# Optimization experiments

Measured on AMD Instinct MI355X. Metric: run time of the kernel, lower is better.

## Reference

```python
import jax, jax.numpy as jnp
import numpy as np

B, N, D = 8, 256, 3          # batch, particles, spatial dims
H = 64                        # hidden_nf (channels)
L = 4                         # num_layers
ENC = 3                       # atom_type, aa_type, aa_pos
IN_NF = ENC + 1               # + time
COORDS_RANGE = 15.0 / L       # tanh=True -> coords_range/n_layers
E = B * N * N                 # fully-connected edges per batch graph


def _linear(key, fin, fout):
    k1, k2 = jax.random.split(key)
    s = 1.0 / np.sqrt(fin)
    w = jax.random.uniform(k1, (fout, fin), minval=-s, maxval=s, dtype=jnp.float32)
    b = jax.random.uniform(k2, (fout,), minval=-s, maxval=s, dtype=jnp.float32)
    return w, b


def setup_inputs() -> dict:
    key = jax.random.key(0)
    ks = jax.random.split(key, 64)
    inp = {
        "t": jax.random.uniform(ks[0], (B, 1), dtype=jnp.float32),
        "x": jax.random.normal(ks[1], (B, N * D), dtype=jnp.float32),
        "atom_type": jax.random.uniform(ks[2], (B, N), dtype=jnp.float32),
        "aa_type": jax.random.uniform(ks[3], (B, N), dtype=jnp.float32),
        "aa_pos": jax.random.uniform(ks[4], (B, N), dtype=jnp.float32),
        "node_mask": jnp.ones((B, N), dtype=jnp.float32),
    }
    inp["emb_w"], inp["emb_b"] = _linear(ks[5], IN_NF, H)
    specs = [("edge_w1", "edge_b1", 2 * H + 2, H), ("edge_w2", "edge_b2", H, H),
             ("node_w1", "node_b1", 2 * H, H), ("node_w2", "node_b2", H, H),
             ("coord_w1", "coord_b1", H, H), ("att_w", "att_b", H, 1)]
    kk = 6
    for wn, bn, fin, fout in specs:
        ws, bs = [], []
        for _ in range(L):
            w, b = _linear(ks[kk], fin, fout); kk += 1
            ws.append(w); bs.append(b)
        inp[wn] = jnp.stack(ws); inp[bn] = jnp.stack(bs)
    # final coord layer: Linear(H,1,bias=False), xavier gain 0.001
    inp["coord_w2"] = jax.random.normal(ks[kk], (L, 1, H), dtype=jnp.float32) * 0.001
    return inp


def _edges():
    idx = jnp.arange(N)
    row_in = jnp.repeat(idx, N)
    col_in = jnp.tile(idx, N)
    off = (jnp.arange(B) * N)[:, None]
    row = (off + row_in[None, :]).reshape(-1)
    col = (off + col_in[None, :]).reshape(-1)
    return row, col


def reference(t, x, atom_type, aa_type, aa_pos, node_mask,
              emb_w, emb_b, edge_w1, edge_b1, edge_w2, edge_b2,
              node_w1, node_b1, node_w2, node_b2,
              coord_w1, coord_b1, att_w, att_b, coord_w2):
    silu = jax.nn.silu
    row, col = _edges()
    nm = node_mask.reshape(B * N, 1)
    # edge mask: pairwise node mask with diagonal (self-loop) removed
    em = ((node_mask[:, :, None] * node_mask[:, None, :])
          * (1.0 - jnp.eye(N, dtype=jnp.float32))).reshape(E, 1)

    x0 = x.reshape(B * N, D) * nm
    tt = jnp.broadcast_to(t, (B, N)).reshape(B * N, 1) * nm
    h = jnp.stack([atom_type, aa_type, aa_pos], axis=-1).reshape(B * N, ENC) * nm
    h = jnp.concatenate([h, tt], axis=1)                      # [BN, 4]
    edge_attr0 = jnp.sum((x0[row] - x0[col]) ** 2, axis=1, keepdims=True)  # [E,1]

    h = h @ emb_w.T + emb_b                                   # embedding -> [BN, H]
    coord = x0
    for l in range(L):
        diff = coord[row] - coord[col]                        # [E, D]
        radial = jnp.sum(diff ** 2, axis=1, keepdims=True)    # [E, 1]
        diff = diff / (jnp.sqrt(radial + 1e-8) + 1.0)         # norm_diff
        m = jnp.concatenate([h[row], h[col], radial, edge_attr0], axis=1)
        m = silu(m @ edge_w1[l].T + edge_b1[l])
        m = silu(m @ edge_w2[l].T + edge_b2[l])               # [E, H]
        m = m * jax.nn.sigmoid(m @ att_w[l].T + att_b[l]) * em
        phi = jnp.tanh(silu(m @ coord_w1[l].T + coord_b1[l]) @ coord_w2[l].T)
        trans = diff * phi * COORDS_RANGE * em                # [E, D]
        coord = (coord + jax.ops.segment_sum(trans, row, num_segments=B * N)) * nm
        agg = jax.ops.segment_sum(m, row, num_segments=B * N)  # [BN, H]
        upd = jnp.concatenate([h, agg], axis=1)
        upd = silu(upd @ node_w1[l].T + node_b1[l]) @ node_w2[l].T + node_b2[l]
        h = (h + upd) * nm                                    # recurrent residual

    vel = (coord - x0) * nm
    vel = vel.reshape(B, N, D)
    nmr = node_mask.reshape(B, N, 1)
    Ns = jnp.sum(nmr, axis=1, keepdims=True)
    vel = vel - (jnp.sum(vel, axis=1, keepdims=True) / Ns) * nmr  # remove_mean_with_mask
    return vel.reshape(B, N * D)
```

## Files before the change

kernel.cpp:

```cpp
#include <hip/hip_runtime.h>

#define CRANGE 3.75f

typedef _Float16 half_t;
typedef __attribute__((ext_vector_type(8))) _Float16 half8;
typedef __attribute__((ext_vector_type(4))) _Float16 half4;
typedef __attribute__((ext_vector_type(4))) float f32x4;

__device__ __forceinline__ float frcp(float x) { return __builtin_amdgcn_rcpf(x); }
__device__ __forceinline__ float fexpn(float x) { return __expf(fminf(x, 20.f)); }
__device__ __forceinline__ float fsilu(float x) { return x * frcp(1.f + fexpn(-x)); }

__device__ __forceinline__ void inv4(float d0, float d1, float d2, float d3, float* o) {
    float p01 = d0 * d1, p23 = d2 * d3;
    float r = frcp(p01 * p23);
    float t01 = p23 * r, t23 = p01 * r;
    o[0] = d1 * t01; o[1] = d0 * t01; o[2] = d3 * t23; o[3] = d2 * t23;
}
__device__ __forceinline__ void silu4(const float* x, float* o) {
    float d0 = 1.f + fexpn(-x[0]), d1 = 1.f + fexpn(-x[1]);
    float d2 = 1.f + fexpn(-x[2]), d3 = 1.f + fexpn(-x[3]);
    float iv[4]; inv4(d0, d1, d2, d3, iv);
    o[0] = x[0] * iv[0]; o[1] = x[1] * iv[1]; o[2] = x[2] * iv[2]; o[3] = x[3] * iv[3];
}

__global__ __launch_bounds__(256) void k_prepinit(
    const float* __restrict__ ew2, const float* __restrict__ cw1,
    const float* __restrict__ nw1, const float* __restrict__ nw2,
    const float* __restrict__ ew1,
    half_t* __restrict__ wf, float* __restrict__ trT,
    const float* __restrict__ t, const float* __restrict__ x,
    const float* __restrict__ at, const float* __restrict__ aa,
    const float* __restrict__ ap, const float* __restrict__ nm,
    const float* __restrict__ embw, const float* __restrict__ embb,
    const float* __restrict__ eb1_0,
    float* __restrict__ h, float* __restrict__ Hr, float* __restrict__ HcA,
    float* __restrict__ x0, float* __restrict__ cA)
{
    if (blockIdx.x < 336) {
        int idx = blockIdx.x * 256 + threadIdx.x;
        if (idx < 4096) {
            int lane = idx & 63;
            int g = (idx >> 6) & 7;
            int mat = (idx >> 9) & 1;
            int l = idx >> 10;
            int mt = g >> 1, kc = g & 1;
            int c = lane & 15, qq = lane >> 4;
            const float* W = (mat ? cw1 : ew2) + l * 4096;
            int row = 16 * mt + c;
            int k0 = 32 * kc + 8 * qq;
            half8 pk;
#pragma unroll
            for (int j = 0; j < 8; ++j) pk[j] = (half_t)W[row * 64 + k0 + j];
            ((half8*)wf)[idx] = pk;
        }
        int tid2 = idx - 4096;
        if (tid2 >= 0 && tid2 < 81920) {
            int l = tid2 / 20480, r = tid2 % 20480;
            float v;
            if (r < 8192)       { int k = r >> 6,        c = r & 63; v = nw1[l * 8192 + c * 128 + k]; }
            else if (r < 12288) { int r2 = r - 8192,  k = r2 >> 6, c = r2 & 63; v = nw2[l * 4096 + c * 64 + k]; }
            else if (r < 16384) { int r2 = r - 12288, k = r2 >> 6, c = r2 & 63; v = ew1[l * 8320 + c * 130 + k]; }
            else                { int r2 = r - 16384, k = r2 >> 6, c = r2 & 63; v = ew1[l * 8320 + c * 130 + 64 + k]; }
            trT[l * 20480 + r] = v;
        }
        return;
    }
    __shared__ float sh[4][64];
    int g = threadIdx.x >> 6, c = threadIdx.x & 63;
    int n = (blockIdx.x - 336) * 4 + g;
    float m = nm[n]; int b = n >> 8;
    float i0 = at[n] * m, i1 = aa[n] * m, i2 = ap[n] * m, i3 = t[b] * m;
    float4 w = ((const float4*)embw)[c];
    float hv = w.x * i0 + w.y * i1 + w.z * i2 + w.w * i3 + embb[c];
    sh[g][c] = hv; h[n * 64 + c] = hv;
    if (c < 3) { float v = x[n * 3 + c] * m; x0[n * 3 + c] = v; cA[n * 3 + c] = v; }
    __syncthreads();
    float a = eb1_0[c], bb = 0.f;
    const float* wa = ew1 + c * 130;
#pragma unroll
    for (int k = 0; k < 64; ++k) {
        float hk = sh[g][k];
        a  += wa[k] * hk;
        bb += wa[64 + k] * hk;
    }
    Hr[n * 64 + c] = a;
    HcA[n * 64 + c] = bb;
}

__global__ __launch_bounds__(256, 4) void k_edge(
    const float* __restrict__ coordIn, const float* __restrict__ x0,
    float* __restrict__ Hr, const float* __restrict__ Hc,
    const float* __restrict__ ew1, const float* __restrict__ eb2,
    const float* __restrict__ cb1, const float* __restrict__ attw,
    const float* __restrict__ attb, const float* __restrict__ cw2,
    const float* __restrict__ nm, const half_t* __restrict__ wf2,
    const half_t* __restrict__ wf1,
    float* __restrict__ hbuf,
    const float* __restrict__ nw1T, const float* __restrict__ nw2T,
    const float* __restrict__ nb1, const float* __restrict__ nb2,
    const float* __restrict__ ew1aTn, const float* __restrict__ ew1bTn,
    const float* __restrict__ eb1n,
    float* __restrict__ HcO, float* __restrict__ coordOut)
{
    __shared__ __align__(16) half_t sV[4][4096];
    __shared__ __align__(16) float sGeo[4][64][4];
    __shared__ float sHr[64], sWr[64], sWe[64], sB2[64], sBc1[64], sAttw[64], sWc2[64];
    __shared__ float sAgg[64];
    __shared__ float sCoord[3];

    const int i = blockIdx.x, b = i >> 8, ir = i & 255;
    const int t = threadIdx.x, wv = t >> 6, e = t & 63;
    const int q = e >> 4, c = e & 15;
    const int col = (b << 8) + t;

    if (t < 64) {
        sHr[t] = Hr[i * 64 + t];
        sWr[t] = ew1[t * 130 + 128];
        sWe[t] = ew1[t * 130 + 129];
        sB2[t] = eb2[t]; sBc1[t] = cb1[t]; sAttw[t] = attw[t]; sWc2[t] = cw2[t];
        sAgg[t] = 0.f;
    }
    if (t == 64) { sCoord[0] = 0.f; sCoord[1] = 0.f; sCoord[2] = 0.f; }
    float attb0 = attb[0];
    float nmi = nm[i];

    float dx = coordIn[i*3+0] - coordIn[col*3+0];
    float dy = coordIn[i*3+1] - coordIn[col*3+1];
    float dz = coordIn[i*3+2] - coordIn[col*3+2];
    float radial = dx*dx + dy*dy + dz*dz;
    float inv = frcp(__builtin_amdgcn_sqrtf(radial + 1e-8f) + 1.f);
    float ex = x0[i*3+0] - x0[col*3+0];
    float ey = x0[i*3+1] - x0[col*3+1];
    float ez = x0[i*3+2] - x0[col*3+2];
    float e0 = ex*ex + ey*ey + ez*ez;
    float em = nmi * nm[col] * ((t == ir) ? 0.f : 1.f);

    __syncthreads();

    {
        float4 g4 = make_float4(dx*inv, dy*inv, dz*inv, em);
        *(float4*)&sGeo[wv][e][0] = g4;
    }

    half_t* mybuf = (half_t*)sV[wv];
    const float4* hcv = (const float4*)(Hc + col * 64);
#pragma unroll
    for (int s = 0; s < 8; ++s) {
        float4 ha = hcv[2*s], hb = hcv[2*s+1];
        float z[8], so[8];
        z[0]=ha.x; z[1]=ha.y; z[2]=ha.z; z[3]=ha.w;
        z[4]=hb.x; z[5]=hb.y; z[6]=hb.z; z[7]=hb.w;
#pragma unroll
        for (int u = 0; u < 8; ++u) {
            int k = 8*s + u;
            z[u] = sHr[k] + z[u] + radial * sWr[k] + e0 * sWe[k];
        }
        silu4(z, so); silu4(z + 4, so + 4);
        half8 pk;
#pragma unroll
        for (int u = 0; u < 8; ++u) pk[u] = (half_t)so[u];
        int f = q * 2 + (s >> 2);
        *(half8*)&mybuf[f * 512 + ((s & 3) * 16 + c) * 8] = pk;
    }

    const half8* bv = (const half8*)mybuf;
    f32x4 acc[4][4];
#pragma unroll
    for (int mt = 0; mt < 4; ++mt) {
        int row0 = 16*mt + 4*q;
#pragma unroll
        for (int nt = 0; nt < 4; ++nt)
#pragma unroll
            for (int r = 0; r < 4; ++r) acc[mt][nt][r] = sB2[row0 + r];
    }
    {
        const half8* a2v = (const half8*)wf2;
        half8 a2[8];
#pragma unroll
        for (int g = 0; g < 8; ++g) a2[g] = a2v[g * 64 + e];
#pragma unroll
        for (int nt = 0; nt < 4; ++nt) {
            half8 b0 = bv[(nt*2+0)*64 + e];
            half8 b1 = bv[(nt*2+1)*64 + e];
#pragma unroll
            for (int mt = 0; mt < 4; ++mt) {
                acc[mt][nt] = __builtin_amdgcn_mfma_f32_16x16x32_f16(a2[mt*2+0], b0, acc[mt][nt], 0, 0, 0);
                acc[mt][nt] = __builtin_amdgcn_mfma_f32_16x16x32_f16(a2[mt*2+1], b1, acc[mt][nt], 0, 0, 0);
            }
        }
    }

    float attp[4] = {0.f, 0.f, 0.f, 0.f};
#pragma unroll
    for (int mt = 0; mt < 4; ++mt) {
        int row0 = 16*mt + 4*q;
#pragma unroll
        for (int nt = 0; nt < 4; ++nt) {
            float z[4], so[4];
#pragma unroll
            for (int r = 0; r < 4; ++r) z[r] = acc[mt][nt][r];
            silu4(z, so);
#pragma unroll
            for (int r = 0; r < 4; ++r) {
                acc[mt][nt][r] = so[r];
                attp[nt] += so[r] * sAttw[row0 + r];
            }
        }
    }
#pragma unroll
    for (int nt = 0; nt < 4; ++nt) {
        float v = attp[nt];
        v += __shfl_xor(v, 16);
        v += __shfl_xor(v, 32);
        attp[nt] = v;
    }
    float scale[4];
    {
        float d0 = 1.f + fexpn(-(attp[0] + attb0));
        float d1 = 1.f + fexpn(-(attp[1] + attb0));
        float d2 = 1.f + fexpn(-(attp[2] + attb0));
        float d3 = 1.f + fexpn(-(attp[3] + attb0));
        float iv[4]; inv4(d0, d1, d2, d3, iv);
#pragma unroll
        for (int nt = 0; nt < 4; ++nt) scale[nt] = iv[nt] * sGeo[wv][16*nt + c][3];
    }

    float aggp[4][4];
#pragma unroll
    for (int mt = 0; mt < 4; ++mt)
#pragma unroll
        for (int r = 0; r < 4; ++r) aggp[mt][r] = 0.f;
#pragma unroll
    for (int mt = 0; mt < 4; ++mt) {
        int kbase = 16*mt + 4*q;
        int fof = ((kbase >> 5) * 512) + (((kbase >> 3) & 3) * 128) + (kbase & 7);
#pragma unroll
        for (int nt = 0; nt < 4; ++nt) {
            half4 pk;
#pragma unroll
            for (int r = 0; r < 4; ++r) {
                float v = acc[mt][nt][r] * scale[nt];
                aggp[mt][r] += v;
                pk[r] = (half_t)v;
            }
            *(half4*)&mybuf[nt*1024 + fof + c*8] = pk;
        }
    }

    half8 a1[8];
    {
        const half8* a1v = (const half8*)wf1;
#pragma unroll
        for (int g = 0; g < 8; ++g) a1[g] = a1v[g * 64 + e];
    }

#pragma unroll
    for (int mt = 0; mt < 4; ++mt)
#pragma unroll
        for (int r = 0; r < 4; ++r) {
            float v = aggp[mt][r];
            v += __shfl_xor(v, 1); v += __shfl_xor(v, 2);
            v += __shfl_xor(v, 4); v += __shfl_xor(v, 8);
            if (c == 0) atomicAdd(&sAgg[16*mt + 4*q + r], v);
        }

    f32x4 acc2[4][4];
#pragma unroll
    for (int mt = 0; mt < 4; ++mt) {
        int row0 = 16*mt + 4*q;
#pragma unroll
        for (int nt = 0; nt < 4; ++nt)
#pragma unroll
            for (int r = 0; r < 4; ++r) acc2[mt][nt][r] = sBc1[row0 + r];
    }
#pragma unroll
    for (int nt = 0; nt < 4; ++nt) {
        half8 b0 = bv[(nt*2+0)*64 + e];
        half8 b1 = bv[(nt*2+1)*64 + e];
#pragma unroll
        for (int mt = 0; mt < 4; ++mt) {
            acc2[mt][nt] = __builtin_amdgcn_mfma_f32_16x16x32_f16(a1[mt*2+0], b0, acc2[mt][nt], 0, 0, 0);
            acc2[mt][nt] = __builtin_amdgcn_mfma_f32_16x16x32_f16(a1[mt*2+1], b1, acc2[mt][nt], 0, 0, 0);
        }
    }

    float php[4] = {0.f, 0.f, 0.f, 0.f};
#pragma unroll
    for (int mt = 0; mt < 4; ++mt) {
        int row0 = 16*mt + 4*q;
#pragma unroll
        for (int nt = 0; nt < 4; ++nt) {
            float z[4], so[4];
#pragma unroll
            for (int r = 0; r < 4; ++r) z[r] = acc2[mt][nt][r];
            silu4(z, so);
#pragma unroll
            for (int r = 0; r < 4; ++r) php[nt] += so[r] * sWc2[row0 + r];
        }
    }
#pragma unroll
    for (int nt = 0; nt < 4; ++nt) {
        float v = php[nt];
        v += __shfl_xor(v, 16);
        v += __shfl_xor(v, 32);
        php[nt] = v;
    }
    float tnh[4];
    {
        float d0 = fexpn(2.f * php[0]) + 1.f;
        float d1 = fexpn(2.f * php[1]) + 1.f;
        float d2 = fexpn(2.f * php[2]) + 1.f;
        float d3 = fexpn(2.f * php[3]) + 1.f;
        float iv[4]; inv4(d0, d1, d2, d3, iv);
#pragma unroll
        for (int nt = 0; nt < 4; ++nt) tnh[nt] = 1.f - 2.f * iv[nt];
    }
    float tx = 0.f, ty = 0.f, tz = 0.f;
#pragma unroll
    for (int nt = 0; nt < 4; ++nt) {
        float4 g4 = *(float4*)&sGeo[wv][16*nt + c][0];
        float tr = tnh[nt] * CRANGE * g4.w;
        tx += g4.x * tr; ty += g4.y * tr; tz += g4.z * tr;
    }
    tx += __shfl_xor(tx, 1); tx += __shfl_xor(tx, 2); tx += __shfl_xor(tx, 4); tx += __shfl_xor(tx, 8);
    ty += __shfl_xor(ty, 1); ty += __shfl_xor(ty, 2); ty += __shfl_xor(ty, 4); ty += __shfl_xor(ty, 8);
    tz += __shfl_xor(tz, 1); tz += __shfl_xor(tz, 2); tz += __shfl_xor(tz, 4); tz += __shfl_xor(tz, 8);
    if (e == 0) {
        atomicAdd(&sCoord[0], tx);
        atomicAdd(&sCoord[1], ty);
        atomicAdd(&sCoord[2], tz);
    }

    __syncthreads();

    float* sT  = (float*)&sV[0][0];
    float* sIn = sT;
    float* sU  = sT + 128;
    float* sHn = sT + 192;

    if (t < 64) sIn[t] = hbuf[i * 64 + t];
    else if (t < 128) sIn[t] = sAgg[t - 64];
    if (t >= 128 && t < 131) {
        int d = t - 128;
        coordOut[i * 3 + d] = (coordIn[i * 3 + d] + sCoord[d]) * nmi;
    }
    __syncthreads();

    const int o = (wv << 4) + c;
    {
        float a = 0.f;
        const float* w = nw1T + (q * 32) * 64 + o;
#pragma unroll
        for (int k = 0; k < 32; ++k) a += w[k * 64] * sIn[q * 32 + k];
        a += __shfl_xor(a, 16);
        a += __shfl_xor(a, 32);
        if (q == 0) sU[o] = fsilu(a + nb1[o]);
    }
    __syncthreads();
    {
        float a = 0.f;
        const float* w = nw2T + (q * 16) * 64 + o;
#pragma unroll
        for (int k = 0; k < 16; ++k) a += w[k * 64] * sU[q * 16 + k];
        a += __shfl_xor(a, 16);
        a += __shfl_xor(a, 32);
        if (q == 0) {
            float hn = (sIn[o] + a + nb2[o]) * nmi;
            hbuf[i * 64 + o] = hn;
            sHn[o] = hn;
        }
    }
    __syncthreads();
    {
        float a = 0.f, bb = 0.f;
        const float* wa = ew1aTn + (q * 16) * 64 + o;
        const float* wb = ew1bTn + (q * 16) * 64 + o;
#pragma unroll
        for (int k = 0; k < 16; ++k) {
            float hv = sHn[q * 16 + k];
            a  += wa[k * 64] * hv;
            bb += wb[k * 64] * hv;
        }
        a  += __shfl_xor(a, 16);  a  += __shfl_xor(a, 32);
        bb += __shfl_xor(bb, 16); bb += __shfl_xor(bb, 32);
        if (q == 0) {
            Hr[i * 64 + o]  = a + eb1n[o];
            HcO[i * 64 + o] = bb;
        }
    }
}

__global__ void k_final(const float* __restrict__ coord, const float* __restrict__ x0,
                        const float* __restrict__ nm, float* __restrict__ out) {
    int b = blockIdx.x;
    int t = threadIdx.x;
    int i = b * 256 + t;
    int lane = t & 63;
    float m = nm[i];
    float vx = (coord[i * 3 + 0] - x0[i * 3 + 0]) * m;
    float vy = (coord[i * 3 + 1] - x0[i * 3 + 1]) * m;
    float vz = (coord[i * 3 + 2] - x0[i * 3 + 2]) * m;
    __shared__ float red[4];
    if (t < 4) red[t] = 0.f;
    __syncthreads();
    float sx = vx, sy = vy, sz = vz, sn = m;
#pragma unroll
    for (int off = 1; off < 64; off <<= 1) {
        sx += __shfl_xor(sx, off);
        sy += __shfl_xor(sy, off);
        sz += __shfl_xor(sz, off);
        sn += __shfl_xor(sn, off);
    }
    if (lane == 0) {
        atomicAdd(&red[0], sx); atomicAdd(&red[1], sy);
        atomicAdd(&red[2], sz); atomicAdd(&red[3], sn);
    }
    __syncthreads();
    float invNs = frcp(red[3]);
    out[b * 768 + t * 3 + 0] = vx - red[0] * invNs * m;
    out[b * 768 + t * 3 + 1] = vy - red[1] * invNs * m;
    out[b * 768 + t * 3 + 2] = vz - red[2] * invNs * m;
}

extern "C" void kernel_launch(void* const* d_in, const int* in_sizes, int n_in,
                              void* d_out, int out_size, void* d_ws, size_t ws_size,
                              hipStream_t stream) {
    const float* t_in    = (const float*)d_in[0];
    const float* x_in    = (const float*)d_in[1];
    const float* at_in   = (const float*)d_in[2];
    const float* aa_in   = (const float*)d_in[3];
    const float* ap_in   = (const float*)d_in[4];
    const float* nm_in   = (const float*)d_in[5];
    const float* emb_w   = (const float*)d_in[6];
    const float* emb_b   = (const float*)d_in[7];
    const float* edge_w1 = (const float*)d_in[8];
    const float* edge_b1 = (const float*)d_in[9];
    const float* edge_w2 = (const float*)d_in[10];
    const float* edge_b2 = (const float*)d_in[11];
    const float* node_w1 = (const float*)d_in[12];
    const float* node_b1 = (const float*)d_in[13];
    const float* node_w2 = (const float*)d_in[14];
    const float* node_b2 = (const float*)d_in[15];
    const float* coord_w1= (const float*)d_in[16];
    const float* coord_b1= (const float*)d_in[17];
    const float* att_w   = (const float*)d_in[18];
    const float* att_b   = (const float*)d_in[19];
    const float* coord_w2= (const float*)d_in[20];

    float* ws  = (float*)d_ws;
    float* h   = ws;
    float* Hr  = h + 131072;
    float* HcA = Hr + 131072;
    float* HcB = HcA + 131072;
    float* x0  = HcB + 131072;
    float* cA  = x0 + 6144;
    float* cB  = cA + 6144;
    float* base = cB + 6144;
    half_t* wf = (half_t*)base;
    float* trT = base + 16384;

    float* out = (float*)d_out;

    k_prepinit<<<848, 256, 0, stream>>>(edge_w2, coord_w1, node_w1, node_w2, edge_w1,
                                        wf, trT,
                                        t_in, x_in, at_in, aa_in, ap_in, nm_in,
                                        emb_w, emb_b, edge_b1,
                                        h, Hr, HcA, x0, cA);

    for (int l = 0; l < 4; ++l) {
        const float* ew1 = edge_w1 + l * 8320;
        const float* eb2 = edge_b2 + l * 64;
        const float* cb1 = coord_b1 + l * 64;
        const float* aw  = att_w + l * 64;
        const float* ab  = att_b + l;
        const float* cw2 = coord_w2 + l * 64;
        const float* nb1 = node_b1 + l * 64;
        const float* nb2 = node_b2 + l * 64;

        const float* trL = trT + l * 20480;
        int ln = (l + 1) & 3;
        const float* trN = trT + ln * 20480;

        const float* cin  = (l & 1) ? cB : cA;
        float*       cout = (l & 1) ? cA : cB;
        const float* HcR  = (l & 1) ? HcB : HcA;
        float*       HcW  = (l & 1) ? HcA : HcB;

        k_edge<<<2048, 256, 0, stream>>>(cin, x0, Hr, HcR, ew1, eb2, cb1,
                                         aw, ab, cw2, nm_in,
                                         wf + l * 8192, wf + l * 8192 + 4096,
                                         h, trL, trL + 8192, nb1, nb2,
                                         trN + 12288, trN + 16384, edge_b1 + ln * 64,
                                         HcW, cout);
    }

    k_final<<<8, 256, 0, stream>>>(cA, x0, nm_in, out);
}
```

Before: 309.6 us.

## Fuse per-layer edge kernels and final reduction into one persistent kernel with grid barriers

Replaces the four per-layer edge launches and the final kernel with one persistent kernel. Its grid is sized from occupancy, it loops over nodes and separates phases with atomic grid barriers. The node update is split out into its own phase after a barrier, with aggregated messages staged through global memory instead of shared memory. The aim is to remove launch overhead between layers. In exchange it adds grid-barrier spin costs and an extra global round trip for agg, and it relies on every block being co-resident to avoid deadlock.

```diff
diff --git a/kernel.cpp b/kernel.cpp
--- a/kernel.cpp
+++ b/kernel.cpp
@@ -24,19 +24,43 @@
     o[0] = x[0] * iv[0]; o[1] = x[1] * iv[1]; o[2] = x[2] * iv[2]; o[3] = x[3] * iv[3];
 }
 
+struct MP {
+    const float* x0; float* cA; float* cB;
+    float* Hr; float* Hc; float* h; float* agg;
+    const float* ew1; const float* eb1; const float* eb2; const float* cb1;
+    const float* attw; const float* attb; const float* cw2; const float* nm;
+    const half_t* wf; const float* trT;
+    const float* nb1; const float* nb2;
+    float* out; int* bar; int nblk;
+};
+
+__device__ __forceinline__ void gridbar(int* cnt, int nblk) {
+    __syncthreads();
+    if (threadIdx.x == 0) {
+        __threadfence();
+        int arrived = __hip_atomic_fetch_add(cnt, 1, __ATOMIC_ACQ_REL, __HIP_MEMORY_SCOPE_AGENT) + 1;
+        if (arrived < nblk) {
+            while (__hip_atomic_load(cnt, __ATOMIC_ACQUIRE, __HIP_MEMORY_SCOPE_AGENT) < nblk)
+                __builtin_amdgcn_s_sleep(2);
+        }
+    }
+    __syncthreads();
+}
+
 __global__ __launch_bounds__(256) void k_prepinit(
     const float* __restrict__ ew2, const float* __restrict__ cw1,
     const float* __restrict__ nw1, const float* __restrict__ nw2,
     const float* __restrict__ ew1,
-    half_t* __restrict__ wf, float* __restrict__ trT,
+    half_t* __restrict__ wf, float* __restrict__ trT, int* __restrict__ bar,
     const float* __restrict__ t, const float* __restrict__ x,
     const float* __restrict__ at, const float* __restrict__ aa,
     const float* __restrict__ ap, const float* __restrict__ nm,
     const float* __restrict__ embw, const float* __restrict__ embb,
     const float* __restrict__ eb1_0,
-    float* __restrict__ h, float* __restrict__ Hr, float* __restrict__ HcA,
+    float* __restrict__ h, float* __restrict__ Hr, float* __restrict__ Hc,
     float* __restrict__ x0, float* __restrict__ cA)
 {
+    if (blockIdx.x == 0 && threadIdx.x < 16) bar[threadIdx.x] = 0;
     if (blockIdx.x < 336) {
         int idx = blockIdx.x * 256 + threadIdx.x;
         if (idx < 4096) {
@@ -85,23 +109,10 @@
         bb += wa[64 + k] * hk;
     }
     Hr[n * 64 + c] = a;
-    HcA[n * 64 + c] = bb;
+    Hc[n * 64 + c] = bb;
 }
 
-__global__ __launch_bounds__(256, 4) void k_edge(
-    const float* __restrict__ coordIn, const float* __restrict__ x0,
-    float* __restrict__ Hr, const float* __restrict__ Hc,
-    const float* __restrict__ ew1, const float* __restrict__ eb2,
-    const float* __restrict__ cb1, const float* __restrict__ attw,
-    const float* __restrict__ attb, const float* __restrict__ cw2,
-    const float* __restrict__ nm, const half_t* __restrict__ wf2,
-    const half_t* __restrict__ wf1,
-    float* __restrict__ hbuf,
-    const float* __restrict__ nw1T, const float* __restrict__ nw2T,
-    const float* __restrict__ nb1, const float* __restrict__ nb2,
-    const float* __restrict__ ew1aTn, const float* __restrict__ ew1bTn,
-    const float* __restrict__ eb1n,
-    float* __restrict__ HcO, float* __restrict__ coordOut)
+__global__ __launch_bounds__(256, 4) void k_mega(MP p)
 {
     __shared__ __align__(16) half_t sV[4][4096];
     __shared__ __align__(16) float sGeo[4][64][4];
@@ -109,318 +120,354 @@
     __shared__ float sAgg[64];
     __shared__ float sCoord[3];
 
-    const int i = blockIdx.x, b = i >> 8, ir = i & 255;
     const int t = threadIdx.x, wv = t >> 6, e = t & 63;
     const int q = e >> 4, c = e & 15;
-    const int col = (b << 8) + t;
-
-    if (t < 64) {
-        sHr[t] = Hr[i * 64 + t];
-        sWr[t] = ew1[t * 130 + 128];
-        sWe[t] = ew1[t * 130 + 129];
-        sB2[t] = eb2[t]; sBc1[t] = cb1[t]; sAttw[t] = attw[t]; sWc2[t] = cw2[t];
-        sAgg[t] = 0.f;
+
+    for (int l = 0; l < 4; ++l) {
+        const float* ew1l = p.ew1 + l * 8320;
+        const float* eb2l = p.eb2 + l * 64;
+        const float* cb1l = p.cb1 + l * 64;
+        const float* awl  = p.attw + l * 64;
+        const float  attb0 = p.attb[l];
+        const float* cw2l = p.cw2 + l * 64;
+        const half_t* wf2 = p.wf + l * 8192;
+        const half_t* wf1 = p.wf + l * 8192 + 4096;
+        const float* coordIn  = (l & 1) ? p.cB : p.cA;
+        float*       coordOut = (l & 1) ? p.cA : p.cB;
+
+        for (int i = blockIdx.x; i < 2048; i += gridDim.x) {
+            const int b = i >> 8, ir = i & 255;
+            const int col = (b << 8) + t;
+
+            if (t < 64) {
+                sHr[t] = p.Hr[i * 64 + t];
+                sWr[t] = ew1l[t * 130 + 128];
+                sWe[t] = ew1l[t * 130 + 129];
+                sB2[t] = eb2l[t]; sBc1[t] = cb1l[t]; sAttw[t] = awl[t]; sWc2[t] = cw2l[t];
+                sAgg[t] = 0.f;
+            }
+            if (t == 64) { sCoord[0] = 0.f; sCoord[1] = 0.f; sCoord[2] = 0.f; }
+            float nmi = p.nm[i];
+
+            float dx = coordIn[i*3+0] - coordIn[col*3+0];
+            float dy = coordIn[i*3+1] - coordIn[col*3+1];
+            float dz = coordIn[i*3+2] - coordIn[col*3+2];
+            float radial = dx*dx + dy*dy + dz*dz;
+            float inv = frcp(__builtin_amdgcn_sqrtf(radial + 1e-8f) + 1.f);
+            float ex = p.x0[i*3+0] - p.x0[col*3+0];
+            float ey = p.x0[i*3+1] - p.x0[col*3+1];
+            float ez = p.x0[i*3+2] - p.x0[col*3+2];
+            float e0 = ex*ex + ey*ey + ez*ez;
+            float em = nmi * p.nm[col] * ((t == ir) ? 0.f : 1.f);
+
+            __syncthreads();
+
+            {
+                float4 g4 = make_float4(dx*inv, dy*inv, dz*inv, em);
+                *(float4*)&sGeo[wv][e][0] = g4;
+            }
+
+            half_t* mybuf = (half_t*)sV[wv];
+            const float4* hcv = (const float4*)(p.Hc + col * 64);
+#pragma unroll
+            for (int s = 0; s < 8; ++s) {
+                float4 ha = hcv[2*s], hb = hcv[2*s+1];
+                float z[8], so[8];
+                z[0]=ha.x; z[1]=ha.y; z[2]=ha.z; z[3]=ha.w;
+                z[4]=hb.x; z[5]=hb.y; z[6]=hb.z; z[7]=hb.w;
+#pragma unroll
+                for (int u = 0; u < 8; ++u) {
+                    int k = 8*s + u;
+                    z[u] = sHr[k] + z[u] + radial * sWr[k] + e0 * sWe[k];
+                }
+                silu4(z, so); silu4(z + 4, so + 4);
+                half8 pk;
+#pragma unroll
+                for (int u = 0; u < 8; ++u) pk[u] = (half_t)so[u];
+                int f = q * 2 + (s >> 2);
+                *(half8*)&mybuf[f * 512 + ((s & 3) * 16 + c) * 8] = pk;
+            }
+
+            const half8* bv = (const half8*)mybuf;
+            f32x4 acc[4][4];
+#pragma unroll
+            for (int mt = 0; mt < 4; ++mt) {
+                int row0 = 16*mt + 4*q;
+#pragma unroll
+                for (int nt = 0; nt < 4; ++nt)
+#pragma unroll
+                    for (int r = 0; r < 4; ++r) acc[mt][nt][r] = sB2[row0 + r];
+            }
+            {
+                const half8* a2v = (const half8*)wf2;
+                half8 a2[8];
+#pragma unroll
+                for (int g = 0; g < 8; ++g) a2[g] = a2v[g * 64 + e];
+#pragma unroll
+                for (int nt = 0; nt < 4; ++nt) {
+                    half8 b0 = bv[(nt*2+0)*64 + e];
+                    half8 b1 = bv[(nt*2+1)*64 + e];
+#pragma unroll
+                    for (int mt = 0; mt < 4; ++mt) {
+                        acc[mt][nt] = __builtin_amdgcn_mfma_f32_16x16x32_f16(a2[mt*2+0], b0, acc[mt][nt], 0, 0, 0);
+                        acc[mt][nt] = __builtin_amdgcn_mfma_f32_16x16x32_f16(a2[mt*2+1], b1, acc[mt][nt], 0, 0, 0);
+                    }
+                }
+            }
+
+            float attp[4] = {0.f, 0.f, 0.f, 0.f};
+#pragma unroll
+            for (int mt = 0; mt < 4; ++mt) {
+                int row0 = 16*mt + 4*q;
+#pragma unroll
+                for (int nt = 0; nt < 4; ++nt) {
+                    float z[4], so[4];
+#pragma unroll
+                    for (int r = 0; r < 4; ++r) z[r] = acc[mt][nt][r];
+                    silu4(z, so);
+#pragma unroll
+                    for (int r = 0; r < 4; ++r) {
+                        acc[mt][nt][r] = so[r];
+                        attp[nt] += so[r] * sAttw[row0 + r];
+                    }
+                }
+            }
+#pragma unroll
+            for (int nt = 0; nt < 4; ++nt) {
+                float v = attp[nt];
+                v += __shfl_xor(v, 16);
+                v += __shfl_xor(v, 32);
+                attp[nt] = v;
+            }
+            float scale[4];
+            {
+                float d0 = 1.f + fexpn(-(attp[0] + attb0));
+                float d1 = 1.f + fexpn(-(attp[1] + attb0));
+                float d2 = 1.f + fexpn(-(attp[2] + attb0));
+                float d3 = 1.f + fexpn(-(attp[3] + attb0));
+                float iv[4]; inv4(d0, d1, d2, d3, iv);
+#pragma unroll
+                for (int nt = 0; nt < 4; ++nt) scale[nt] = iv[nt] * sGeo[wv][16*nt + c][3];
+            }
+
+            float aggp[4][4];
+#pragma unroll
+            for (int mt = 0; mt < 4; ++mt)
+#pragma unroll
+                for (int r = 0; r < 4; ++r) aggp[mt][r] = 0.f;
+#pragma unroll
+            for (int mt = 0; mt < 4; ++mt) {
+                int kbase = 16*mt + 4*q;
+                int fof = ((kbase >> 5) * 512) + (((kbase >> 3) & 3) * 128) + (kbase & 7);
+#pragma unroll
+                for (int nt = 0; nt < 4; ++nt) {
+                    half4 pk;
+#pragma unroll
+                    for (int r = 0; r < 4; ++r) {
+                        float v = acc[mt][nt][r] * scale[nt];
+                        aggp[mt][r] += v;
+                        pk[r] = (half_t)v;
+                    }
+                    *(half4*)&mybuf[nt*1024 + fof + c*8] = pk;
+                }
+            }
+
+            half8 a1[8];
+            {
+                const half8* a1v = (const half8*)wf1;
+#pragma unroll
+                for (int g = 0; g < 8; ++g) a1[g] = a1v[g * 64 + e];
+            }
+
+#pragma unroll
+            for (int mt = 0; mt < 4; ++mt)
+#pragma unroll
+                for (int r = 0; r < 4; ++r) {
+                    float v = aggp[mt][r];
+                    v += __shfl_xor(v, 1); v += __shfl_xor(v, 2);
+                    v += __shfl_xor(v, 4); v += __shfl_xor(v, 8);
+                    if (c == 0) atomicAdd(&sAgg[16*mt + 4*q + r], v);
+                }
+
+            f32x4 acc2[4][4];
+#pragma unroll
+            for (int mt = 0; mt < 4; ++mt) {
+                int row0 = 16*mt + 4*q;
+#pragma unroll
+                for (int nt = 0; nt < 4; ++nt)
+#pragma unroll
+                    for (int r = 0; r < 4; ++r) acc2[mt][nt][r] = sBc1[row0 + r];
+            }
+#pragma unroll
+            for (int nt = 0; nt < 4; ++nt) {
+                half8 b0 = bv[(nt*2+0)*64 + e];
+                half8 b1 = bv[(nt*2+1)*64 + e];
+#pragma unroll
+                for (int mt = 0; mt < 4; ++mt) {
+                    acc2[mt][nt] = __builtin_amdgcn_mfma_f32_16x16x32_f16(a1[mt*2+0], b0, acc2[mt][nt], 0, 0, 0);
+                    acc2[mt][nt] = __builtin_amdgcn_mfma_f32_16x16x32_f16(a1[mt*2+1], b1, acc2[mt][nt], 0, 0, 0);
+                }
+            }
+
+            float php[4] = {0.f, 0.f, 0.f, 0.f};
+#pragma unroll
+            for (int mt = 0; mt < 4; ++mt) {
+                int row0 = 16*mt + 4*q;
+#pragma unroll
+                for (int nt = 0; nt < 4; ++nt) {
+                    float z[4], so[4];
+#pragma unroll
+                    for (int r = 0; r < 4; ++r) z[r] = acc2[mt][nt][r];
+                    silu4(z, so);
+#pragma unroll
+                    for (int r = 0; r < 4; ++r) php[nt] += so[r] * sWc2[row0 + r];
+                }
+            }
+#pragma unroll
+            for (int nt = 0; nt < 4; ++nt) {
+                float v = php[nt];
+                v += __shfl_xor(v, 16);
+                v += __shfl_xor(v, 32);
+                php[nt] = v;
+            }
+            float tnh[4];
+            {
+                float d0 = fexpn(2.f * php[0]) + 1.f;
+                float d1 = fexpn(2.f * php[1]) + 1.f;
+                float d2 = fexpn(2.f * php[2]) + 1.f;
+                float d3 = fexpn(2.f * php[3]) + 1.f;
+                float iv[4]; inv4(d0, d1, d2, d3, iv);
+#pragma unroll
+                for (int nt = 0; nt < 4; ++nt) tnh[nt] = 1.f - 2.f * iv[nt];
+            }
+            float tx = 0.f, ty = 0.f, tz = 0.f;
+#pragma unroll
+            for (int nt = 0; nt < 4; ++nt) {
+                float4 g4 = *(float4*)&sGeo[wv][16*nt + c][0];
+                float tr = tnh[nt] * CRANGE * g4.w;
+                tx += g4.x * tr; ty += g4.y * tr; tz += g4.z * tr;
+            }
+            tx += __shfl_xor(tx, 1); tx += __shfl_xor(tx, 2); tx += __shfl_xor(tx, 4); tx += __shfl_xor(tx, 8);
+            ty += __shfl_xor(ty, 1); ty += __shfl_xor(ty, 2); ty += __shfl_xor(ty, 4); ty += __shfl_xor(ty, 8);
+            tz += __shfl_xor(tz, 1); tz += __shfl_xor(tz, 2); tz += __shfl_xor(tz, 4); tz += __shfl_xor(tz, 8);
+            if (e == 0) {
+                atomicAdd(&sCoord[0], tx);
+                atomicAdd(&sCoord[1], ty);
+                atomicAdd(&sCoord[2], tz);
+            }
+
+            __syncthreads();
+            if (t < 64) p.agg[i * 64 + t] = sAgg[t];
+            if (t >= 64 && t < 67) {
+                int d = t - 64;
+                coordOut[i * 3 + d] = (coordIn[i * 3 + d] + sCoord[d]) * nmi;
+            }
+            __syncthreads();
+        }
+
+        gridbar(p.bar + 2 * l, p.nblk);
+
+        if (l < 3) {
+            const float* trL = p.trT + l * 20480;
+            const float* trN = p.trT + (l + 1) * 20480;
+            const float* nw1T = trL;
+            const float* nw2T = trL + 8192;
+            const float* e1aT = trN + 12288;
+            const float* e1bT = trN + 16384;
+            const float* nb1l = p.nb1 + l * 64;
+            const float* nb2l = p.nb2 + l * 64;
+            const float* eb1n = p.eb1 + (l + 1) * 64;
+
+            float* sT  = (float*)&sV[0][0];
+            float* sIn = sT;
+            float* sP  = sT + 128;
+            float* sU  = sT + 384;
+            float* sHn = sT + 448;
+            float* sPB = sT + 512;
+            const int cc = t & 63, pp = t >> 6;
+
+            for (int n = blockIdx.x; n < 2048; n += gridDim.x) {
+                float nmi = p.nm[n];
+                if (t < 64) sIn[t] = p.h[n * 64 + t];
+                else if (t < 128) sIn[t] = p.agg[n * 64 + t - 64];
+                __syncthreads();
+                {
+                    float a = 0.f;
+                    const float* w = nw1T + (pp * 32) * 64 + cc;
+#pragma unroll
+                    for (int k = 0; k < 32; ++k) a += w[k * 64] * sIn[pp * 32 + k];
+                    sP[pp * 64 + cc] = a;
+                }
+                __syncthreads();
+                if (t < 64) sU[t] = fsilu(sP[t] + sP[64 + t] + sP[128 + t] + sP[192 + t] + nb1l[t]);
+                __syncthreads();
+                {
+                    float a = 0.f;
+                    const float* w = nw2T + (pp * 16) * 64 + cc;
+#pragma unroll
+                    for (int k = 0; k < 16; ++k) a += w[k * 64] * sU[pp * 16 + k];
+                    sP[pp * 64 + cc] = a;
+                }
+                __syncthreads();
+                if (t < 64) {
+                    float hn = (sIn[t] + sP[t] + sP[64 + t] + sP[128 + t] + sP[192 + t] + nb2l[t]) * nmi;
+                    p.h[n * 64 + t] = hn;
+                    sHn[t] = hn;
+                }
+                __syncthreads();
+                {
+                    float a = 0.f, b2 = 0.f;
+                    const float* wa = e1aT + (pp * 16) * 64 + cc;
+                    const float* wb = e1bT + (pp * 16) * 64 + cc;
+#pragma unroll
+                    for (int k = 0; k < 16; ++k) {
+                        float hv = sHn[pp * 16 + k];
+                        a  += wa[k * 64] * hv;
+                        b2 += wb[k * 64] * hv;
+                    }
+                    sP[pp * 64 + cc] = a;
+                    sPB[pp * 64 + cc] = b2;
+                }
+                __syncthreads();
+                if (t < 64) {
+                    p.Hr[n * 64 + t] = sP[t] + sP[64 + t] + sP[128 + t] + sP[192 + t] + eb1n[t];
+                    p.Hc[n * 64 + t] = sPB[t] + sPB[64 + t] + sPB[128 + t] + sPB[192 + t];
+                }
+                __syncthreads();
+            }
+            gridbar(p.bar + 2 * l + 1, p.nblk);
+        }
     }
-    if (t == 64) { sCoord[0] = 0.f; sCoord[1] = 0.f; sCoord[2] = 0.f; }
-    float attb0 = attb[0];
-    float nmi = nm[i];
-
-    float dx = coordIn[i*3+0] - coordIn[col*3+0];
-    float dy = coordIn[i*3+1] - coordIn[col*3+1];
-    float dz = coordIn[i*3+2] - coordIn[col*3+2];
-    float radial = dx*dx + dy*dy + dz*dz;
-    float inv = frcp(__builtin_amdgcn_sqrtf(radial + 1e-8f) + 1.f);
-    float ex = x0[i*3+0] - x0[col*3+0];
-    float ey = x0[i*3+1] - x0[col*3+1];
-    float ez = x0[i*3+2] - x0[col*3+2];
-    float e0 = ex*ex + ey*ey + ez*ez;
-    float em = nmi * nm[col] * ((t == ir) ? 0.f : 1.f);
-
-    __syncthreads();
-
-    {
-        float4 g4 = make_float4(dx*inv, dy*inv, dz*inv, em);
-        *(float4*)&sGeo[wv][e][0] = g4;
+
+    if (blockIdx.x < 8) {
+        float* red = (float*)&sV[0][0];
+        int b = blockIdx.x;
+        int i = b * 256 + t;
+        int lane = t & 63;
+        float m = p.nm[i];
+        float vx = (p.cA[i * 3 + 0] - p.x0[i * 3 + 0]) * m;
+        float vy = (p.cA[i * 3 + 1] - p.x0[i * 3 + 1]) * m;
+        float vz = (p.cA[i * 3 + 2] - p.x0[i * 3 + 2]) * m;
+        if (t < 4) red[t] = 0.f;
+        __syncthreads();
+        float sx = vx, sy = vy, sz = vz, sn = m;
+#pragma unroll
+        for (int off = 1; off < 64; off <<= 1) {
+            sx += __shfl_xor(sx, off);
+            sy += __shfl_xor(sy, off);
+            sz += __shfl_xor(sz, off);
+            sn += __shfl_xor(sn, off);
+        }
+        if (lane == 0) {
+            atomicAdd(&red[0], sx); atomicAdd(&red[1], sy);
+            atomicAdd(&red[2], sz); atomicAdd(&red[3], sn);
+        }
+        __syncthreads();
+        float invNs = frcp(red[3]);
+        p.out[b * 768 + t * 3 + 0] = vx - red[0] * invNs * m;
+        p.out[b * 768 + t * 3 + 1] = vy - red[1] * invNs * m;
+        p.out[b * 768 + t * 3 + 2] = vz - red[2] * invNs * m;
     }
-
-    half_t* mybuf = (half_t*)sV[wv];
-    const float4* hcv = (const float4*)(Hc + col * 64);
-#pragma unroll
-    for (int s = 0; s < 8; ++s) {
-        float4 ha = hcv[2*s], hb = hcv[2*s+1];
-        float z[8], so[8];
-        z[0]=ha.x; z[1]=ha.y; z[2]=ha.z; z[3]=ha.w;
-        z[4]=hb.x; z[5]=hb.y; z[6]=hb.z; z[7]=hb.w;
-#pragma unroll
-        for (int u = 0; u < 8; ++u) {
-            int k = 8*s + u;
-            z[u] = sHr[k] + z[u] + radial * sWr[k] + e0 * sWe[k];
-        }
-        silu4(z, so); silu4(z + 4, so + 4);
-        half8 pk;
-#pragma unroll
-        for (int u = 0; u < 8; ++u) pk[u] = (half_t)so[u];
-        int f = q * 2 + (s >> 2);
-        *(half8*)&mybuf[f * 512 + ((s & 3) * 16 + c) * 8] = pk;
-    }
-
-    const half8* bv = (const half8*)mybuf;
-    f32x4 acc[4][4];
-#pragma unroll
-    for (int mt = 0; mt < 4; ++mt) {
-        int row0 = 16*mt + 4*q;
-#pragma unroll
-        for (int nt = 0; nt < 4; ++nt)
-#pragma unroll
-            for (int r = 0; r < 4; ++r) acc[mt][nt][r] = sB2[row0 + r];
-    }
-    {
-        const half8* a2v = (const half8*)wf2;
-        half8 a2[8];
-#pragma unroll
-        for (int g = 0; g < 8; ++g) a2[g] = a2v[g * 64 + e];
-#pragma unroll
-        for (int nt = 0; nt < 4; ++nt) {
-            half8 b0 = bv[(nt*2+0)*64 + e];
-            half8 b1 = bv[(nt*2+1)*64 + e];
-#pragma unroll
-            for (int mt = 0; mt < 4; ++mt) {
-                acc[mt][nt] = __builtin_amdgcn_mfma_f32_16x16x32_f16(a2[mt*2+0], b0, acc[mt][nt], 0, 0, 0);
-                acc[mt][nt] = __builtin_amdgcn_mfma_f32_16x16x32_f16(a2[mt*2+1], b1, acc[mt][nt], 0, 0, 0);
-            }
-        }
-    }
-
-    float attp[4] = {0.f, 0.f, 0.f, 0.f};
-#pragma unroll
-    for (int mt = 0; mt < 4; ++mt) {
-        int row0 = 16*mt + 4*q;
-#pragma unroll
-        for (int nt = 0; nt < 4; ++nt) {
-            float z[4], so[4];
-#pragma unroll
-            for (int r = 0; r < 4; ++r) z[r] = acc[mt][nt][r];
-            silu4(z, so);
-#pragma unroll
-            for (int r = 0; r < 4; ++r) {
-                acc[mt][nt][r] = so[r];
-                attp[nt] += so[r] * sAttw[row0 + r];
-            }
-        }
-    }
-#pragma unroll
-    for (int nt = 0; nt < 4; ++nt) {
-        float v = attp[nt];
-        v += __shfl_xor(v, 16);
-        v += __shfl_xor(v, 32);
-        attp[nt] = v;
-    }
-    float scale[4];
-    {
-        float d0 = 1.f + fexpn(-(attp[0] + attb0));
-        float d1 = 1.f + fexpn(-(attp[1] + attb0));
-        float d2 = 1.f + fexpn(-(attp[2] + attb0));
-        float d3 = 1.f + fexpn(-(attp[3] + attb0));
-        float iv[4]; inv4(d0, d1, d2, d3, iv);
-#pragma unroll
-        for (int nt = 0; nt < 4; ++nt) scale[nt] = iv[nt] * sGeo[wv][16*nt + c][3];
-    }
-
-    float aggp[4][4];
-#pragma unroll
-    for (int mt = 0; mt < 4; ++mt)
-#pragma unroll
-        for (int r = 0; r < 4; ++r) aggp[mt][r] = 0.f;
-#pragma unroll
-    for (int mt = 0; mt < 4; ++mt) {
-        int kbase = 16*mt + 4*q;
-        int fof = ((kbase >> 5) * 512) + (((kbase >> 3) & 3) * 128) + (kbase & 7);
-#pragma unroll
-        for (int nt = 0; nt < 4; ++nt) {
-            half4 pk;
-#pragma unroll
-            for (int r = 0; r < 4; ++r) {
-                float v = acc[mt][nt][r] * scale[nt];
-                aggp[mt][r] += v;
-                pk[r] = (half_t)v;
-            }
-            *(half4*)&mybuf[nt*1024 + fof + c*8] = pk;
-        }
-    }
-
-    half8 a1[8];
-    {
-        const half8* a1v = (const half8*)wf1;
-#pragma unroll
-        for (int g = 0; g < 8; ++g) a1[g] = a1v[g * 64 + e];
-    }
-
-#pragma unroll
-    for (int mt = 0; mt < 4; ++mt)
-#pragma unroll
-        for (int r = 0; r < 4; ++r) {
-            float v = aggp[mt][r];
-            v += __shfl_xor(v, 1); v += __shfl_xor(v, 2);
-            v += __shfl_xor(v, 4); v += __shfl_xor(v, 8);
-            if (c == 0) atomicAdd(&sAgg[16*mt + 4*q + r], v);
-        }
-
-    f32x4 acc2[4][4];
-#pragma unroll
-    for (int mt = 0; mt < 4; ++mt) {
-        int row0 = 16*mt + 4*q;
-#pragma unroll
-        for (int nt = 0; nt < 4; ++nt)
-#pragma unroll
-            for (int r = 0; r < 4; ++r) acc2[mt][nt][r] = sBc1[row0 + r];
-    }
-#pragma unroll
-    for (int nt = 0; nt < 4; ++nt) {
-        half8 b0 = bv[(nt*2+0)*64 + e];
-        half8 b1 = bv[(nt*2+1)*64 + e];
-#pragma unroll
-        for (int mt = 0; mt < 4; ++mt) {
-            acc2[mt][nt] = __builtin_amdgcn_mfma_f32_16x16x32_f16(a1[mt*2+0], b0, acc2[mt][nt], 0, 0, 0);
-            acc2[mt][nt] = __builtin_amdgcn_mfma_f32_16x16x32_f16(a1[mt*2+1], b1, acc2[mt][nt], 0, 0, 0);
-        }
-    }
-
-    float php[4] = {0.f, 0.f, 0.f, 0.f};
-#pragma unroll
-    for (int mt = 0; mt < 4; ++mt) {
-        int row0 = 16*mt + 4*q;
-#pragma unroll
-        for (int nt = 0; nt < 4; ++nt) {
-            float z[4], so[4];
-#pragma unroll
-            for (int r = 0; r < 4; ++r) z[r] = acc2[mt][nt][r];
-            silu4(z, so);
-#pragma unroll
-            for (int r = 0; r < 4; ++r) php[nt] += so[r] * sWc2[row0 + r];
-        }
-    }
-#pragma unroll
-    for (int nt = 0; nt < 4; ++nt) {
-        float v = php[nt];
-        v += __shfl_xor(v, 16);
-        v += __shfl_xor(v, 32);
-        php[nt] = v;
-    }
-    float tnh[4];
-    {
-        float d0 = fexpn(2.f * php[0]) + 1.f;
-        float d1 = fexpn(2.f * php[1]) + 1.f;
-        float d2 = fexpn(2.f * php[2]) + 1.f;
-        float d3 = fexpn(2.f * php[3]) + 1.f;
-        float iv[4]; inv4(d0, d1, d2, d3, iv);
-#pragma unroll
-        for (int nt = 0; nt < 4; ++nt) tnh[nt] = 1.f - 2.f * iv[nt];
-    }
-    float tx = 0.f, ty = 0.f, tz = 0.f;
-#pragma unroll
-    for (int nt = 0; nt < 4; ++nt) {
-        float4 g4 = *(float4*)&sGeo[wv][16*nt + c][0];
-        float tr = tnh[nt] * CRANGE * g4.w;
-        tx += g4.x * tr; ty += g4.y * tr; tz += g4.z * tr;
-    }
-    tx += __shfl_xor(tx, 1); tx += __shfl_xor(tx, 2); tx += __shfl_xor(tx, 4); tx += __shfl_xor(tx, 8);
-    ty += __shfl_xor(ty, 1); ty += __shfl_xor(ty, 2); ty += __shfl_xor(ty, 4); ty += __shfl_xor(ty, 8);
-    tz += __shfl_xor(tz, 1); tz += __shfl_xor(tz, 2); tz += __shfl_xor(tz, 4); tz += __shfl_xor(tz, 8);
-    if (e == 0) {
-        atomicAdd(&sCoord[0], tx);
-        atomicAdd(&sCoord[1], ty);
-        atomicAdd(&sCoord[2], tz);
-    }
-
-    __syncthreads();
-
-    float* sT  = (float*)&sV[0][0];
-    float* sIn = sT;
-    float* sU  = sT + 128;
-    float* sHn = sT + 192;
-
-    if (t < 64) sIn[t] = hbuf[i * 64 + t];
-    else if (t < 128) sIn[t] = sAgg[t - 64];
-    if (t >= 128 && t < 131) {
-        int d = t - 128;
-        coordOut[i * 3 + d] = (coordIn[i * 3 + d] + sCoord[d]) * nmi;
-    }
-    __syncthreads();
-
-    const int o = (wv << 4) + c;
-    {
-        float a = 0.f;
-        const float* w = nw1T + (q * 32) * 64 + o;
-#pragma unroll
-        for (int k = 0; k < 32; ++k) a += w[k * 64] * sIn[q * 32 + k];
-        a += __shfl_xor(a, 16);
-        a += __shfl_xor(a, 32);
-        if (q == 0) sU[o] = fsilu(a + nb1[o]);
-    }
-    __syncthreads();
-    {
-        float a = 0.f;
-        const float* w = nw2T + (q * 16) * 64 + o;
-#pragma unroll
-        for (int k = 0; k < 16; ++k) a += w[k * 64] * sU[q * 16 + k];
-        a += __shfl_xor(a, 16);
-        a += __shfl_xor(a, 32);
-        if (q == 0) {
-            float hn = (sIn[o] + a + nb2[o]) * nmi;
-            hbuf[i * 64 + o] = hn;
-            sHn[o] = hn;
-        }
-    }
-    __syncthreads();
-    {
-        float a = 0.f, bb = 0.f;
-        const float* wa = ew1aTn + (q * 16) * 64 + o;
-        const float* wb = ew1bTn + (q * 16) * 64 + o;
-#pragma unroll
-        for (int k = 0; k < 16; ++k) {
-            float hv = sHn[q * 16 + k];
-            a  += wa[k * 64] * hv;
-            bb += wb[k * 64] * hv;
-        }
-        a  += __shfl_xor(a, 16);  a  += __shfl_xor(a, 32);
-        bb += __shfl_xor(bb, 16); bb += __shfl_xor(bb, 32);
-        if (q == 0) {
-            Hr[i * 64 + o]  = a + eb1n[o];
-            HcO[i * 64 + o] = bb;
-        }
-    }
-}
-
-__global__ void k_final(const float* __restrict__ coord, const float* __restrict__ x0,
-                        const float* __restrict__ nm, float* __restrict__ out) {
-    int b = blockIdx.x;
-    int t = threadIdx.x;
-    int i = b * 256 + t;
-    int lane = t & 63;
-    float m = nm[i];
-    float vx = (coord[i * 3 + 0] - x0[i * 3 + 0]) * m;
-    float vy = (coord[i * 3 + 1] - x0[i * 3 + 1]) * m;
-    float vz = (coord[i * 3 + 2] - x0[i * 3 + 2]) * m;
-    __shared__ float red[4];
-    if (t < 4) red[t] = 0.f;
-    __syncthreads();
-    float sx = vx, sy = vy, sz = vz, sn = m;
-#pragma unroll
-    for (int off = 1; off < 64; off <<= 1) {
-        sx += __shfl_xor(sx, off);
-        sy += __shfl_xor(sy, off);
-        sz += __shfl_xor(sz, off);
-        sn += __shfl_xor(sn, off);
-    }
-    if (lane == 0) {
-        atomicAdd(&red[0], sx); atomicAdd(&red[1], sy);
-        atomicAdd(&red[2], sz); atomicAdd(&red[3], sn);
-    }
-    __syncthreads();
-    float invNs = frcp(red[3]);
-    out[b * 768 + t * 3 + 0] = vx - red[0] * invNs * m;
-    out[b * 768 + t * 3 + 1] = vy - red[1] * invNs * m;
-    out[b * 768 + t * 3 + 2] = vz - red[2] * invNs * m;
 }
 
 extern "C" void kernel_launch(void* const* d_in, const int* in_sizes, int n_in,
@@ -451,49 +498,39 @@
     float* ws  = (float*)d_ws;
     float* h   = ws;
     float* Hr  = h + 131072;
-    float* HcA = Hr + 131072;
-    float* HcB = HcA + 131072;
-    float* x0  = HcB + 131072;
+    float* Hc  = Hr + 131072;
+    float* agg = Hc + 131072;
+    float* x0  = agg + 131072;
     float* cA  = x0 + 6144;
     float* cB  = cA + 6144;
     float* base = cB + 6144;
     half_t* wf = (half_t*)base;
     float* trT = base + 16384;
+    int*   bar = (int*)(trT + 81920);
 
     float* out = (float*)d_out;
 
     k_prepinit<<<848, 256, 0, stream>>>(edge_w2, coord_w1, node_w1, node_w2, edge_w1,
-                                        wf, trT,
+                                        wf, trT, bar,
                                         t_in, x_in, at_in, aa_in, ap_in, nm_in,
                                         emb_w, emb_b, edge_b1,
-                                        h, Hr, HcA, x0, cA);
-
-    for (int l = 0; l < 4; ++l) {
-        const float* ew1 = edge_w1 + l * 8320;
-        const float* eb2 = edge_b2 + l * 64;
-        const float* cb1 = coord_b1 + l * 64;
-        const float* aw  = att_w + l * 64;
-        const float* ab  = att_b + l;
-        const float* cw2 = coord_w2 + l * 64;
-        const float* nb1 = node_b1 + l * 64;
-        const float* nb2 = node_b2 + l * 64;
-
-        const float* trL = trT + l * 20480;
-        int ln = (l + 1) & 3;
-        const float* trN = trT + ln * 20480;
-
-        const float* cin  = (l & 1) ? cB : cA;
-        float*       cout = (l & 1) ? cA : cB;
-        const float* HcR  = (l & 1) ? HcB : HcA;
-        float*       HcW  = (l & 1) ? HcA : HcB;
-
-        k_edge<<<2048, 256, 0, stream>>>(cin, x0, Hr, HcR, ew1, eb2, cb1,
-                                         aw, ab, cw2, nm_in,
-                                         wf + l * 8192, wf + l * 8192 + 4096,
-                                         h, trL, trL + 8192, nb1, nb2,
-                                         trN + 12288, trN + 16384, edge_b1 + ln * 64,
-                                         HcW, cout);
-    }
-
-    k_final<<<8, 256, 0, stream>>>(cA, x0, nm_in, out);
+                                        h, Hr, Hc, x0, cA);
+
+    int maxB = 0;
+    (void)hipOccupancyMaxActiveBlocksPerMultiprocessor(&maxB, k_mega, 256, 0);
+    if (maxB < 1) maxB = 1;
+    if (maxB > 8) maxB = 8;
+    int grid = maxB * 256;
+    if (grid > 2048) grid = 2048;
+
+    MP p;
+    p.x0 = x0; p.cA = cA; p.cB = cB;
+    p.Hr = Hr; p.Hc = Hc; p.h = h; p.agg = agg;
+    p.ew1 = edge_w1; p.eb1 = edge_b1; p.eb2 = edge_b2; p.cb1 = coord_b1;
+    p.attw = att_w; p.attb = att_b; p.cw2 = coord_w2; p.nm = nm_in;
+    p.wf = wf; p.trT = trT;
+    p.nb1 = node_b1; p.nb2 = node_b2;
+    p.out = out; p.bar = bar; p.nblk = grid;
+
+    k_mega<<<grid, 256, 0, stream>>>(p);
 }
```

Measured after the change: 924.2 us. +198.5%, slower.
